# Performance work log

Measured on AMD Instinct MI355X. Metric: run time of the kernel, lower is better.

Reference implementation:

```python
import jax, jax.numpy as jnp
import numpy as np
import math

IN_C, OUT_C, K, STYLE_DIM = 512, 512, 3, 512
BATCH, H, W = 16, 64, 64
EPS = 1e-8
CONV_SCALE = 1.0 / math.sqrt(IN_C * K * K)   # fan_in scale
MOD_SCALE = 1.0 / math.sqrt(STYLE_DIM)       # EqualLinear scale (lr_mul=1)


def setup_inputs() -> dict:
    key = jax.random.key(0)
    k1, k2, k3, k4 = jax.random.split(key, 4)
    return {
        "input": jax.random.normal(k1, (BATCH, IN_C, H, W), dtype=jnp.float32),
        "style": jax.random.normal(k2, (BATCH, STYLE_DIM), dtype=jnp.float32),
        "weight": jax.random.normal(k3, (1, OUT_C, IN_C, K, K), dtype=jnp.float32),
        "mod_weight": jax.random.normal(k4, (IN_C, STYLE_DIM), dtype=jnp.float32),
        "mod_bias": jnp.ones((IN_C,), dtype=jnp.float32),  # bias_init=1
    }


def reference(input, style, weight, mod_weight, mod_bias):
    b = input.shape[0]
    # EqualLinear modulation: style -> per-sample per-in-channel scale
    s = style @ (mod_weight * MOD_SCALE).T + mod_bias          # [B, IN_C]
    # Modulate base weight per sample
    w = CONV_SCALE * weight * s[:, None, :, None, None]        # [B, OUT_C, IN_C, K, K]
    # Demodulation
    demod = jax.lax.rsqrt(jnp.sum(w * w, axis=(2, 3, 4)) + EPS)  # [B, OUT_C]
    w = w * demod[:, :, None, None, None]
    # Grouped conv with groups=batch == per-sample conv; vmap over batch
    pad = K // 2

    def conv_one(x, wk):
        # x: [IN_C, H, W], wk: [OUT_C, IN_C, K, K]
        y = jax.lax.conv_general_dilated(
            x[None], wk, window_strides=(1, 1),
            padding=[(pad, pad), (pad, pad)],
            dimension_numbers=("NCHW", "OIHW", "NCHW"))
        return y[0]

    out = jax.vmap(conv_one)(input, w)                          # [B, OUT_C, H, W]
    return out
```

## Files before the change

kernel.cpp:

```cpp
#include <hip/hip_runtime.h>

#define IN_C 512
#define OUT_C 512
#define BATCH 16
#define NPX 4096

using bf16x8 = __attribute__((ext_vector_type(8))) __bf16;
using f32x4  = __attribute__((ext_vector_type(4))) float;

static constexpr float kConvScale = 0.014731391274719739f;
static constexpr float kModScale  = 0.04419417382415922f;
static constexpr float kEps       = 1e-8f;

#define WT_TILE_BYTES (9 * 128 * 64)

__global__ void style_k(const float* __restrict__ style, const float* __restrict__ mw,
                        const float* __restrict__ mb, float* __restrict__ s) {
  __shared__ float st[IN_C];
  const int b = blockIdx.x, t = threadIdx.x;
  st[t] = style[b * IN_C + t];
  __syncthreads();
  const float4* row = (const float4*)(mw + (size_t)t * IN_C);
  float acc = 0.f;
  #pragma unroll 4
  for (int i = 0; i < IN_C / 4; i++) {
    float4 v = row[i];
    float4 u = *(const float4*)(st + i * 4);
    acc += v.x * u.x + v.y * u.y + v.z * u.z + v.w * u.w;
  }
  s[b * IN_C + t] = acc * kModScale + mb[t];
}

__global__ void wprep_k(const float* __restrict__ w, float* __restrict__ wsq,
                        char* __restrict__ wsw) {
  const int idx = blockIdx.x * 256 + threadIdx.x;
  const int ic = idx & (IN_C - 1), oc = idx >> 9;
  const int ot = oc >> 7, ocl = oc & 127, ics = ic >> 5, icl = ic & 31;
  char* tile = wsw + (size_t)(ics * 4 + ot) * WT_TILE_BYTES;
  const float* p = w + (size_t)(oc * IN_C + ic) * 9;
  float q = 0.f;
  #pragma unroll
  for (int t = 0; t < 9; t++) {
    float v = p[t];
    q += v * v;
    int B = ((t * 128 + ocl) << 6) + icl * 2;
    int Bsw = B ^ (((B >> 7) & 7) << 4);
    *(__bf16*)(tile + Bsw) = (__bf16)v;
  }
  wsq[oc * IN_C + ic] = q;
}

__global__ void demod_k(const float* __restrict__ s, const float* __restrict__ wsq,
                        float* __restrict__ dsc) {
  __shared__ float s2[IN_C];
  const int b = blockIdx.x, t = threadIdx.x;
  float sv = s[b * IN_C + t];
  s2[t] = sv * sv;
  __syncthreads();
  const float4* row = (const float4*)(wsq + (size_t)t * IN_C);
  float acc = 0.f;
  #pragma unroll 4
  for (int i = 0; i < IN_C / 4; i++) {
    float4 v = row[i];
    float4 u = *(const float4*)(s2 + i * 4);
    acc += v.x * u.x + v.y * u.y + v.z * u.z + v.w * u.w;
  }
  dsc[b * OUT_C + t] = kConvScale * rsqrtf(kConvScale * kConvScale * acc + kEps);
}

__global__ void modx_k(const float* __restrict__ x, const float* __restrict__ s,
                       __bf16* __restrict__ xm) {
  __shared__ __bf16 tile[64][73];
  const int t = threadIdx.x;
  const int bid = blockIdx.x;
  const int ict = bid & 7, pt = (bid >> 3) & 63, b = bid >> 9;
  const int ic0 = ict * 64, p0 = pt * 64;
  #pragma unroll
  for (int it = 0; it < 16; it++) {
    int idx = it * 256 + t;
    int pl = idx & 63, icl = idx >> 6;
    int ic = ic0 + icl;
    float v = x[((size_t)b * IN_C + ic) * NPX + p0 + pl] * s[b * IN_C + ic];
    tile[icl][pl] = (__bf16)v;
  }
  __syncthreads();
  #pragma unroll
  for (int it = 0; it < 2; it++) {
    int idx = it * 256 + t;
    int icb = idx & 7, pl = idx >> 3;
    alignas(16) __bf16 tmp[8];
    #pragma unroll
    for (int j = 0; j < 8; j++) tmp[j] = tile[icb * 8 + j][pl];
    *(uint4*)(xm + ((size_t)b * NPX + p0 + pl) * IN_C + ic0 + icb * 8) = *(const uint4*)tmp;
  }
}

#define ICP 40

#define SGB __builtin_amdgcn_sched_group_barrier
#define SGB_MIX() { SGB(0x100, 3, 0); SGB(0x8, 8, 0); SGB(0x100, 3, 0); SGB(0x8, 8, 0); \
                    SGB(0x100, 3, 0); SGB(0x8, 8, 0); SGB(0x100, 3, 0); SGB(0x8, 8, 0); }
#define SGB_MFMA() { SGB(0x8, 8, 0); SGB(0x8, 8, 0); SGB(0x8, 8, 0); SGB(0x8, 8, 0); }

__global__ __launch_bounds__(512, 2)
void conv_k(const __bf16* __restrict__ xm, const char* __restrict__ wsw,
            const float* __restrict__ dsc, float* __restrict__ out) {
  __shared__ __align__(16) __bf16 xs[10][66][ICP];
  __shared__ uint4 wsb4[WT_TILE_BYTES / 16];
  char* wsb = (char*)wsb4;

  const int tid = threadIdx.x;
  const int lane = tid & 63;
  const int wv = tid >> 6;
  const int wm = wv >> 2, wn = wv & 3;
  const int l15 = lane & 15, kb8 = lane >> 4;
  const int bid = blockIdx.x;
  const int pt = bid & 7, ot = (bid >> 3) & 3, b = bid >> 5;
  const int h0 = pt * 8, oc0 = ot * 128;

  if (tid < 80) {
    int ckb = tid & 3, side = (tid >> 2) & 1, r = tid >> 3;
    uint4 z = {0, 0, 0, 0};
    *(uint4*)(&xs[r][side * 65][ckb * 8]) = z;
  }

  const int s_ckb = tid & 3, s_c = (tid >> 2) & 63, s_rb = tid >> 8;
  const __bf16* xbase = xm + (size_t)b * NPX * IN_C + s_c * IN_C + s_ckb * 8;

  uint4 ld[5];
  #define LOADX(ICS)                                                          \
    {                                                                         \
      _Pragma("unroll")                                                       \
      for (int it = 0; it < 5; it++) {                                        \
        int r = it * 2 + s_rb;                                                \
        int h = h0 + r - 1;                                                   \
        uint4 v = {0, 0, 0, 0};                                               \
        if ((unsigned)h < 64u)                                                \
          v = *(const uint4*)(xbase + (size_t)h * 64 * IN_C + (ICS) * 32);    \
        ld[it] = v;                                                           \
      }                                                                       \
    }
  #define WRITEX()                                                            \
    {                                                                         \
      _Pragma("unroll")                                                       \
      for (int it = 0; it < 5; it++) {                                        \
        int r = it * 2 + s_rb;                                                \
        *(uint4*)(&xs[r][s_c + 1][s_ckb * 8]) = ld[it];                       \
      }                                                                       \
    }
  #define LOADW(ICS)                                                          \
    {                                                                         \
      const char* wt = wsw + (size_t)((ICS) * 4 + ot) * WT_TILE_BYTES;        \
      _Pragma("unroll")                                                       \
      for (int it = 0; it < 9; it++) {                                        \
        int off = (it * 512 + tid) * 16;                                      \
        __builtin_amdgcn_global_load_lds(                                     \
            (const __attribute__((address_space(1))) void*)(wt + off),        \
            (__attribute__((address_space(3))) void*)(wsb + off), 16, 0, 0);  \
      }                                                                       \
    }

  f32x4 acc[4][8];
  #pragma unroll
  for (int i = 0; i < 4; i++)
    #pragma unroll
    for (int j = 0; j < 8; j++) acc[i][j] = f32x4{0.f, 0.f, 0.f, 0.f};

  const int ocr_base = wm * 64 + l15;
  const int swz = ((l15 >> 1) & 7) << 4;
  const int wrd_base = ((ocr_base << 6) + kb8 * 16) ^ swz;

  bf16x8 afA[4], bfA[8], afB[4], bfB[8];
  #define LOADT(T, AF, BF)                                                    \
    {                                                                         \
      _Pragma("unroll")                                                       \
      for (int fm = 0; fm < 4; fm++)                                          \
        AF[fm] = *(const bf16x8*)(wsb + ((T) * 8192 + fm * 1024 + wrd_base)); \
      _Pragma("unroll")                                                       \
      for (int fn = 0; fn < 8; fn++) {                                        \
        int px = wn * 128 + fn * 16 + l15;                                    \
        BF[fn] = *(const bf16x8*)(&xs[(px >> 6) + ((T) / 3)]                  \
                                     [(px & 63) + ((T) % 3)]                  \
                                     [kb8 * 8]);                              \
      }                                                                       \
    }
  #define MFMAT(AF, BF)                                                       \
    {                                                                         \
      _Pragma("unroll")                                                       \
      for (int fm = 0; fm < 4; fm++)                                          \
        _Pragma("unroll")                                                     \
        for (int fn = 0; fn < 8; fn++)                                        \
          acc[fm][fn] = __builtin_amdgcn_mfma_f32_16x16x32_bf16(              \
              AF[fm], BF[fn], acc[fm][fn], 0, 0, 0);                          \
    }

  LOADX(0)

  for (int s = 0; s < 16; s++) {
    __syncthreads();
    LOADW(s)
    WRITEX()
    __syncthreads();
    if (s < 15) LOADX(s + 1)

    LOADT(0, afA, bfA)
    LOADT(1, afB, bfB)
    MFMAT(afA, bfA)  SGB_MIX()
    LOADT(2, afA, bfA)
    MFMAT(afB, bfB)  SGB_MIX()
    LOADT(3, afB, bfB)
    MFMAT(afA, bfA)  SGB_MIX()
    LOADT(4, afA, bfA)
    MFMAT(afB, bfB)  SGB_MIX()
    LOADT(5, afB, bfB)
    MFMAT(afA, bfA)  SGB_MIX()
    LOADT(6, afA, bfA)
    MFMAT(afB, bfB)  SGB_MIX()
    LOADT(7, afB, bfB)
    MFMAT(afA, bfA)  SGB_MIX()
    LOADT(8, afA, bfA)
    MFMAT(afB, bfB)  SGB_MIX()
    MFMAT(afA, bfA)  SGB_MFMA()
  }

  #pragma unroll
  for (int fm = 0; fm < 4; fm++) {
    #pragma unroll
    for (int j = 0; j < 4; j++) {
      int oc = oc0 + wm * 64 + fm * 16 + kb8 * 4 + j;
      float dm = dsc[b * OUT_C + oc];
      float* orow = out + ((size_t)b * OUT_C + oc) * NPX + h0 * 64;
      #pragma unroll
      for (int fn = 0; fn < 8; fn++) {
        int px = wn * 128 + fn * 16 + l15;
        orow[px] = acc[fm][fn][j] * dm;
      }
    }
  }
}

extern "C" void kernel_launch(void* const* d_in, const int* in_sizes, int n_in,
                              void* d_out, int out_size, void* d_ws, size_t ws_size,
                              hipStream_t stream) {
  const float* input  = (const float*)d_in[0];
  const float* style  = (const float*)d_in[1];
  const float* weight = (const float*)d_in[2];
  const float* mod_w  = (const float*)d_in[3];
  const float* mod_b  = (const float*)d_in[4];
  float* out = (float*)d_out;

  char* p = (char*)d_ws;
  float* s    = (float*)p;  p += (size_t)BATCH * IN_C * 4;
  float* dsc  = (float*)p;  p += (size_t)BATCH * OUT_C * 4;
  float* wsq  = (float*)p;  p += (size_t)OUT_C * IN_C * 4;
  char*  wsw  = p;          p += (size_t)16 * 4 * WT_TILE_BYTES;
  __bf16* xm  = (__bf16*)p;

  style_k<<<BATCH, 512, 0, stream>>>(style, mod_w, mod_b, s);
  wprep_k<<<1024, 256, 0, stream>>>(weight, wsq, wsw);
  demod_k<<<BATCH, 512, 0, stream>>>(s, wsq, dsc);
  modx_k<<<BATCH * 8 * 64, 256, 0, stream>>>(input, s, xm);
  conv_k<<<BATCH * 4 * 8, 512, 0, stream>>>(xm, wsw, dsc, out);
}
```

Measured before the change: 343.2 us.

## Pipeline conv main loop with split weight loads, double-buffered swizzled input tile

Restructures the conv K-loop so that the weight tile is fetched in three thirds, interleaved with the three kernel-row groups. The input tile is double-buffered inside 128-byte channel rows, using an XOR half-select and a swizzled chunk placement to avoid LDS bank conflicts. Explicit vmcnt waits and raw barriers replace __syncthreads, and s_setprio raises priority around MFMA blocks. Halo rows are zeroed once and the loads are clamped, which removes the branches from the global load path. This aims to overlap global/LDS traffic with MFMA work, at the cost of delicate hand-counted waitcnt correctness.

```diff
diff --git a/kernel.cpp b/kernel.cpp
--- a/kernel.cpp
+++ b/kernel.cpp
@@ -95,18 +95,27 @@
   }
 }
 
-#define ICP 40
 
 #define SGB __builtin_amdgcn_sched_group_barrier
 #define SGB_MIX() { SGB(0x100, 3, 0); SGB(0x8, 8, 0); SGB(0x100, 3, 0); SGB(0x8, 8, 0); \
                     SGB(0x100, 3, 0); SGB(0x8, 8, 0); SGB(0x100, 3, 0); SGB(0x8, 8, 0); }
 #define SGB_MFMA() { SGB(0x8, 8, 0); SGB(0x8, 8, 0); SGB(0x8, 8, 0); SGB(0x8, 8, 0); }
 
+#define WAITV(N) asm volatile("s_waitcnt vmcnt(" #N ")" ::: "memory")
+#define WAITL()  asm volatile("s_waitcnt lgkmcnt(0)" ::: "memory")
+#define SBAR()   { __builtin_amdgcn_sched_barrier(0); __builtin_amdgcn_s_barrier(); \
+                   __builtin_amdgcn_sched_barrier(0); }
+#define PRIO1()  __builtin_amdgcn_s_setprio(1)
+#define PRIO0()  __builtin_amdgcn_s_setprio(0)
+
+__device__ __forceinline__ int swz8(int u) { return 4 * (u & 1) + ((u >> 1) & 3); }
+
 __global__ __launch_bounds__(512, 2)
 void conv_k(const __bf16* __restrict__ xm, const char* __restrict__ wsw,
             const float* __restrict__ dsc, float* __restrict__ out) {
-  __shared__ __align__(16) __bf16 xs[10][66][ICP];
+  __shared__ __align__(16) char xsb_s[10 * 66 * 128];
   __shared__ uint4 wsb4[WT_TILE_BYTES / 16];
+  char* xsb = xsb_s;
   char* wsb = (char*)wsb4;
 
   const int tid = threadIdx.x;
@@ -114,18 +123,18 @@
   const int wv = tid >> 6;
   const int wm = wv >> 2, wn = wv & 3;
   const int l15 = lane & 15, kb8 = lane >> 4;
+  const int l7 = l15 & 7;
   const int bid = blockIdx.x;
   const int pt = bid & 7, ot = (bid >> 3) & 3, b = bid >> 5;
   const int h0 = pt * 8, oc0 = ot * 128;
 
-  if (tid < 80) {
-    int ckb = tid & 3, side = (tid >> 2) & 1, r = tid >> 3;
-    uint4 z = {0, 0, 0, 0};
-    *(uint4*)(&xs[r][side * 65][ckb * 8]) = z;
-  }
-
   const int s_ckb = tid & 3, s_c = (tid >> 2) & 63, s_rb = tid >> 8;
   const __bf16* xbase = xm + (size_t)b * NPX * IN_C + s_c * IN_C + s_ckb * 8;
+
+  const int rp_0 = ((kb8 + swz8((l7 + 7) & 7)) & 7) * 16;
+  const int rp_1 = ((kb8 + swz8(l7)) & 7) * 16;
+  const int rp_2 = ((kb8 + swz8((l7 + 1) & 7)) & 7) * 16;
+  const int wpb  = ((s_ckb + swz8(s_c & 7)) & 7) * 16;
 
   uint4 ld[5];
   #define LOADX(ICS)                                                          \
@@ -134,26 +143,26 @@
       for (int it = 0; it < 5; it++) {                                        \
         int r = it * 2 + s_rb;                                                \
         int h = h0 + r - 1;                                                   \
-        uint4 v = {0, 0, 0, 0};                                               \
-        if ((unsigned)h < 64u)                                                \
-          v = *(const uint4*)(xbase + (size_t)h * 64 * IN_C + (ICS) * 32);    \
-        ld[it] = v;                                                           \
+        int hc = h < 0 ? 0 : (h > 63 ? 63 : h);                               \
+        ld[it] = *(const uint4*)(xbase + (size_t)hc * 64 * IN_C + (ICS) * 32);\
       }                                                                       \
     }
-  #define WRITEX()                                                            \
+  #define WRITEX(WP)                                                          \
     {                                                                         \
       _Pragma("unroll")                                                       \
       for (int it = 0; it < 5; it++) {                                        \
         int r = it * 2 + s_rb;                                                \
-        *(uint4*)(&xs[r][s_c + 1][s_ckb * 8]) = ld[it];                       \
+        int h = h0 + r - 1;                                                   \
+        if ((unsigned)h < 64u)                                                \
+          *(uint4*)(xsb + r * 8448 + (s_c + 1) * 128 + (WP)) = ld[it];        \
       }                                                                       \
     }
-  #define LOADW(ICS)                                                          \
+  #define LOADW_G(ICS, G)                                                     \
     {                                                                         \
       const char* wt = wsw + (size_t)((ICS) * 4 + ot) * WT_TILE_BYTES;        \
       _Pragma("unroll")                                                       \
-      for (int it = 0; it < 9; it++) {                                        \
-        int off = (it * 512 + tid) * 16;                                      \
+      for (int it = 0; it < 3; it++) {                                        \
+        int off = (((G) * 3 + it) * 512 + tid) * 16;                          \
         __builtin_amdgcn_global_load_lds(                                     \
             (const __attribute__((address_space(1))) void*)(wt + off),        \
             (__attribute__((address_space(3))) void*)(wsb + off), 16, 0, 0);  \
@@ -170,19 +179,24 @@
   const int swz = ((l15 >> 1) & 7) << 4;
   const int wrd_base = ((ocr_base << 6) + kb8 * 16) ^ swz;
 
+  int xoff[8];
+  #pragma unroll
+  for (int fn = 0; fn < 8; fn++) {
+    int px = wn * 128 + fn * 16 + l15;
+    xoff[fn] = (px >> 6) * 8448 + (px & 63) * 128;
+  }
+
   bf16x8 afA[4], bfA[8], afB[4], bfB[8];
   #define LOADT(T, AF, BF)                                                    \
     {                                                                         \
       _Pragma("unroll")                                                       \
       for (int fm = 0; fm < 4; fm++)                                          \
         AF[fm] = *(const bf16x8*)(wsb + ((T) * 8192 + fm * 1024 + wrd_base)); \
-      _Pragma("unroll")                                                       \
-      for (int fn = 0; fn < 8; fn++) {                                        \
-        int px = wn * 128 + fn * 16 + l15;                                    \
-        BF[fn] = *(const bf16x8*)(&xs[(px >> 6) + ((T) / 3)]                  \
-                                     [(px & 63) + ((T) % 3)]                  \
-                                     [kb8 * 8]);                              \
-      }                                                                       \
+      const int cdx_ = (T) % 3 == 0 ? c0 : ((T) % 3 == 1 ? c1 : c2);          \
+      _Pragma("unroll")                                                       \
+      for (int fn = 0; fn < 8; fn++)                                          \
+        BF[fn] = *(const bf16x8*)(xsb + xoff[fn] + ((T) / 3) * 8448 +         \
+                                  ((T) % 3) * 128 + cdx_);                    \
     }
   #define MFMAT(AF, BF)                                                       \
     {                                                                         \
@@ -193,35 +207,52 @@
           acc[fm][fn] = __builtin_amdgcn_mfma_f32_16x16x32_bf16(              \
               AF[fm], BF[fn], acc[fm][fn], 0, 0, 0);                          \
     }
-
+  #define GROUP3(T0)                                                          \
+    LOADT(T0 + 0, afA, bfA)                                                   \
+    LOADT(T0 + 1, afB, bfB)                                                   \
+    PRIO1(); MFMAT(afA, bfA); PRIO0(); SGB_MIX()                              \
+    LOADT(T0 + 2, afA, bfA)                                                   \
+    PRIO1(); MFMAT(afB, bfB); PRIO0(); SGB_MIX()                              \
+    PRIO1(); MFMAT(afA, bfA); PRIO0(); SGB_MFMA()
+
+  {
+    uint4 z = {0, 0, 0, 0};
+    if (tid < 160) {
+      int r = tid >> 4, side = (tid >> 3) & 1, ch = tid & 7;
+      *(uint4*)(xsb + r * 8448 + side * 65 * 128 + ch * 16) = z;
+    }
+    if (h0 == 0)
+      for (int i = tid; i < 528; i += 512) ((uint4*)xsb)[i] = z;
+    if (h0 == 56)
+      for (int i = tid; i < 528; i += 512) ((uint4*)(xsb + 9 * 8448))[i] = z;
+  }
   LOADX(0)
+  LOADW_G(0, 0)
+  LOADW_G(0, 1)
+  WAITV(0);
+  WRITEX(wpb)
 
   for (int s = 0; s < 16; s++) {
-    __syncthreads();
-    LOADW(s)
-    WRITEX()
-    __syncthreads();
-    if (s < 15) LOADX(s + 1)
-
-    LOADT(0, afA, bfA)
-    LOADT(1, afB, bfB)
-    MFMAT(afA, bfA)  SGB_MIX()
-    LOADT(2, afA, bfA)
-    MFMAT(afB, bfB)  SGB_MIX()
-    LOADT(3, afB, bfB)
-    MFMAT(afA, bfA)  SGB_MIX()
-    LOADT(4, afA, bfA)
-    MFMAT(afB, bfB)  SGB_MIX()
-    LOADT(5, afB, bfB)
-    MFMAT(afA, bfA)  SGB_MIX()
-    LOADT(6, afA, bfA)
-    MFMAT(afB, bfB)  SGB_MIX()
-    LOADT(7, afB, bfB)
-    MFMAT(afA, bfA)  SGB_MIX()
-    LOADT(8, afA, bfA)
-    MFMAT(afB, bfB)  SGB_MIX()
-    MFMAT(afA, bfA)  SGB_MFMA()
-  }
+    const int sn = s < 15 ? s + 1 : 15;
+    const int hh = (s & 1) << 6;
+    const int c0 = rp_0 ^ hh, c1 = rp_1 ^ hh, c2 = rp_2 ^ hh;
+    const int wp = wpb ^ hh ^ 64;
+
+    WAITV(3); WAITL(); SBAR();
+    LOADX(sn)
+    LOADW_G(s, 2)
+    GROUP3(0)
+
+    WAITV(8); SBAR();
+    LOADW_G(sn, 0)
+    GROUP3(3)
+
+    WAITV(3); SBAR();
+    WRITEX(wp)
+    LOADW_G(sn, 1)
+    GROUP3(6)
+  }
+  WAITV(0);
 
   #pragma unroll
   for (int fm = 0; fm < 4; fm++) {
```

Result: slower. 502.0 us (+46.3%).

## Use 4-wave blocks with 128x128 per-wave tiles and double-buffered async input loads

Applied to the files above, without the earlier changes.

The conv block drops from 8 to 4 waves, and each wave now computes all 128 output channels over 128 pixels (acc 8x8 fragments), which doubles register accumulator use and A-fragment reuse. The input tile now goes straight into LDS with global_load_lds into two buffers, with zeroed halo rows, replacing the register staging path. This removes the register round trip and its write barrier. In exchange it roughly doubles LDS use, keeps one block per CU with heavy VGPR pressure, and halves the wave count available to hide latency. The weight tile is still loaded synchronously, under barriers, at each step.

```diff
diff --git a/kernel.cpp b/kernel.cpp
--- a/kernel.cpp
+++ b/kernel.cpp
@@ -95,113 +95,120 @@
   }
 }
 
-#define ICP 40
+
+#define XROW 4224
+#define XBUF 42240
 
 #define SGB __builtin_amdgcn_sched_group_barrier
-#define SGB_MIX() { SGB(0x100, 3, 0); SGB(0x8, 8, 0); SGB(0x100, 3, 0); SGB(0x8, 8, 0); \
-                    SGB(0x100, 3, 0); SGB(0x8, 8, 0); SGB(0x100, 3, 0); SGB(0x8, 8, 0); }
-#define SGB_MFMA() { SGB(0x8, 8, 0); SGB(0x8, 8, 0); SGB(0x8, 8, 0); SGB(0x8, 8, 0); }
-
-__global__ __launch_bounds__(512, 2)
+#define SGB_MIX() { SGB(0x100, 2, 0); SGB(0x8, 8, 0); SGB(0x100, 2, 0); SGB(0x8, 8, 0); \
+                    SGB(0x100, 2, 0); SGB(0x8, 8, 0); SGB(0x100, 2, 0); SGB(0x8, 8, 0); \
+                    SGB(0x100, 2, 0); SGB(0x8, 8, 0); SGB(0x100, 2, 0); SGB(0x8, 8, 0); \
+                    SGB(0x100, 2, 0); SGB(0x8, 8, 0); SGB(0x100, 2, 0); SGB(0x8, 8, 0); }
+#define SGB_MFMA() { SGB(0x8, 8, 0); SGB(0x8, 8, 0); SGB(0x8, 8, 0); SGB(0x8, 8, 0); \
+                     SGB(0x8, 8, 0); SGB(0x8, 8, 0); SGB(0x8, 8, 0); SGB(0x8, 8, 0); }
+
+__global__ __launch_bounds__(256, 1)
 void conv_k(const __bf16* __restrict__ xm, const char* __restrict__ wsw,
             const float* __restrict__ dsc, float* __restrict__ out) {
-  __shared__ __align__(16) __bf16 xs[10][66][ICP];
-  __shared__ uint4 wsb4[WT_TILE_BYTES / 16];
-  char* wsb = (char*)wsb4;
+  __shared__ __align__(16) char xsb[2 * XBUF];
+  __shared__ __align__(16) char wsb[WT_TILE_BYTES];
 
   const int tid = threadIdx.x;
   const int lane = tid & 63;
-  const int wv = tid >> 6;
-  const int wm = wv >> 2, wn = wv & 3;
+  const int wn = tid >> 6;
   const int l15 = lane & 15, kb8 = lane >> 4;
   const int bid = blockIdx.x;
   const int pt = bid & 7, ot = (bid >> 3) & 3, b = bid >> 5;
   const int h0 = pt * 8, oc0 = ot * 128;
 
-  if (tid < 80) {
-    int ckb = tid & 3, side = (tid >> 2) & 1, r = tid >> 3;
+  if (tid < 160) {
+    int bb = tid / 80, rr = (tid % 80) >> 3, side = (tid >> 2) & 1, ch = tid & 3;
     uint4 z = {0, 0, 0, 0};
-    *(uint4*)(&xs[r][side * 65][ckb * 8]) = z;
-  }
-
-  const int s_ckb = tid & 3, s_c = (tid >> 2) & 63, s_rb = tid >> 8;
-  const __bf16* xbase = xm + (size_t)b * NPX * IN_C + s_c * IN_C + s_ckb * 8;
-
-  uint4 ld[5];
-  #define LOADX(ICS)                                                          \
-    {                                                                         \
-      _Pragma("unroll")                                                       \
-      for (int it = 0; it < 5; it++) {                                        \
-        int r = it * 2 + s_rb;                                                \
+    *(uint4*)(xsb + bb * XBUF + rr * XROW + side * 65 * 64 + ch * 16) = z;
+  }
+  if (h0 == 0) {
+    uint4 z = {0, 0, 0, 0};
+    for (int i = tid; i < 2 * 264; i += 256)
+      *((uint4*)(xsb + (i >= 264 ? XBUF : 0)) + (i % 264)) = z;
+  }
+  if (h0 == 56) {
+    uint4 z = {0, 0, 0, 0};
+    for (int i = tid; i < 2 * 264; i += 256)
+      *((uint4*)(xsb + (i >= 264 ? XBUF : 0) + 9 * XROW) + (i % 264)) = z;
+  }
+
+  #define XGLDS(ICS, BUF)                                                     \
+    {                                                                         \
+      _Pragma("unroll")                                                       \
+      for (int r = 0; r < 10; r++) {                                          \
         int h = h0 + r - 1;                                                   \
-        uint4 v = {0, 0, 0, 0};                                               \
         if ((unsigned)h < 64u)                                                \
-          v = *(const uint4*)(xbase + (size_t)h * 64 * IN_C + (ICS) * 32);    \
-        ld[it] = v;                                                           \
+          __builtin_amdgcn_global_load_lds(                                   \
+              (const __attribute__((address_space(1))) void*)(xm +            \
+                  ((size_t)(b * 4096 + h * 64 + (tid >> 2))) * 512 +          \
+                  (ICS) * 32 + (tid & 3) * 8),                                \
+              (__attribute__((address_space(3))) void*)(xsb + (BUF) +         \
+                  r * XROW + 64 + tid * 16),                                  \
+              16, 0, 0);                                                      \
       }                                                                       \
     }
-  #define WRITEX()                                                            \
-    {                                                                         \
-      _Pragma("unroll")                                                       \
-      for (int it = 0; it < 5; it++) {                                        \
-        int r = it * 2 + s_rb;                                                \
-        *(uint4*)(&xs[r][s_c + 1][s_ckb * 8]) = ld[it];                       \
-      }                                                                       \
-    }
-  #define LOADW(ICS)                                                          \
+  #define WGLDS(ICS)                                                          \
     {                                                                         \
       const char* wt = wsw + (size_t)((ICS) * 4 + ot) * WT_TILE_BYTES;        \
       _Pragma("unroll")                                                       \
-      for (int it = 0; it < 9; it++) {                                        \
-        int off = (it * 512 + tid) * 16;                                      \
+      for (int g = 0; g < 18; g++) {                                          \
+        int off = (g * 256 + tid) * 16;                                       \
         __builtin_amdgcn_global_load_lds(                                     \
             (const __attribute__((address_space(1))) void*)(wt + off),        \
             (__attribute__((address_space(3))) void*)(wsb + off), 16, 0, 0);  \
       }                                                                       \
     }
 
-  f32x4 acc[4][8];
-  #pragma unroll
-  for (int i = 0; i < 4; i++)
+  f32x4 acc[8][8];
+  #pragma unroll
+  for (int i = 0; i < 8; i++)
     #pragma unroll
     for (int j = 0; j < 8; j++) acc[i][j] = f32x4{0.f, 0.f, 0.f, 0.f};
 
-  const int ocr_base = wm * 64 + l15;
   const int swz = ((l15 >> 1) & 7) << 4;
-  const int wrd_base = ((ocr_base << 6) + kb8 * 16) ^ swz;
-
-  bf16x8 afA[4], bfA[8], afB[4], bfB[8];
+  const int wrd_base = ((l15 << 6) + kb8 * 16) ^ swz;
+
+  int xoff[8];
+  #pragma unroll
+  for (int fn = 0; fn < 8; fn++) {
+    int px = wn * 128 + fn * 16 + l15;
+    xoff[fn] = (px >> 6) * XROW + (px & 63) * 64 + kb8 * 16;
+  }
+
+  bf16x8 afA[8], bfA[8], afB[8], bfB[8];
   #define LOADT(T, AF, BF)                                                    \
     {                                                                         \
       _Pragma("unroll")                                                       \
-      for (int fm = 0; fm < 4; fm++)                                          \
+      for (int fm = 0; fm < 8; fm++)                                          \
         AF[fm] = *(const bf16x8*)(wsb + ((T) * 8192 + fm * 1024 + wrd_base)); \
       _Pragma("unroll")                                                       \
-      for (int fn = 0; fn < 8; fn++) {                                        \
-        int px = wn * 128 + fn * 16 + l15;                                    \
-        BF[fn] = *(const bf16x8*)(&xs[(px >> 6) + ((T) / 3)]                  \
-                                     [(px & 63) + ((T) % 3)]                  \
-                                     [kb8 * 8]);                              \
-      }                                                                       \
+      for (int fn = 0; fn < 8; fn++)                                          \
+        BF[fn] = *(const bf16x8*)(xcur + xoff[fn] + ((T) / 3) * XROW +        \
+                                  ((T) % 3) * 64);                            \
     }
   #define MFMAT(AF, BF)                                                       \
     {                                                                         \
       _Pragma("unroll")                                                       \
-      for (int fm = 0; fm < 4; fm++)                                          \
+      for (int fm = 0; fm < 8; fm++)                                          \
         _Pragma("unroll")                                                     \
         for (int fn = 0; fn < 8; fn++)                                        \
           acc[fm][fn] = __builtin_amdgcn_mfma_f32_16x16x32_bf16(              \
               AF[fm], BF[fn], acc[fm][fn], 0, 0, 0);                          \
     }
 
-  LOADX(0)
+  XGLDS(0, 0)
 
   for (int s = 0; s < 16; s++) {
+    const char* xcur = xsb + (s & 1) * XBUF;
     __syncthreads();
-    LOADW(s)
-    WRITEX()
+    WGLDS(s)
     __syncthreads();
-    if (s < 15) LOADX(s + 1)
+    if (s < 15) XGLDS(s + 1, ((s + 1) & 1) * XBUF)
 
     LOADT(0, afA, bfA)
     LOADT(1, afB, bfB)
@@ -224,10 +231,10 @@
   }
 
   #pragma unroll
-  for (int fm = 0; fm < 4; fm++) {
+  for (int fm = 0; fm < 8; fm++) {
     #pragma unroll
     for (int j = 0; j < 4; j++) {
-      int oc = oc0 + wm * 64 + fm * 16 + kb8 * 4 + j;
+      int oc = oc0 + fm * 16 + kb8 * 4 + j;
       float dm = dsc[b * OUT_C + oc];
       float* orow = out + ((size_t)b * OUT_C + oc) * NPX + h0 * 64;
       #pragma unroll
@@ -260,5 +267,5 @@
   wprep_k<<<1024, 256, 0, stream>>>(weight, wsq, wsw);
   demod_k<<<BATCH, 512, 0, stream>>>(s, wsq, dsc);
   modx_k<<<BATCH * 8 * 64, 256, 0, stream>>>(input, s, xm);
-  conv_k<<<BATCH * 4 * 8, 512, 0, stream>>>(xm, wsw, dsc, out);
-}
+  conv_k<<<BATCH * 4 * 8, 256, 0, stream>>>(xm, wsw, dsc, out);
+}
```

Measured after the change: 606.6 us. 76.7% more time.
